# Kernel tuning notes

Hardware: AMD Instinct MI355X
Metric: run time of the kernel (lower is better)

Reference implementation:

```python
import jax, jax.numpy as jnp
import numpy as np

WIDTH, HEIGHT = 96, 72
DIST_COEF = 0.1  # CARLA

# CARLA intrinsics per options_from_source: fx=fy=cx=width/2, cy=height/2
_K = np.array([[48.0, 48.0, 0.0], [36.0, 0.0, 36.0], [1.0, 0.0, 0.0]], dtype=np.float64)
_invK = np.linalg.inv(_K)
_u = np.arange(WIDTH, dtype=np.float64)
_v = np.arange(HEIGHT, dtype=np.float64)
_uu = np.tile(_u, (HEIGHT, 1)).reshape(-1)
_vv = np.repeat(_v, WIDTH)
_uv1 = np.stack([_uu, _vv, np.ones_like(_uu)], axis=0)  # (3, N)
YZ1_GRID = jnp.asarray((_invK @ _uv1).astype(np.float32))  # (3, N)


def setup_inputs() -> dict:
    key = jax.random.key(0)
    k1, k2, k3, k4, k5, k6 = jax.random.split(key, 6)
    B = 1
    # depths strictly positive so the depth>0 mask keeps every pixel (dense, jit-friendly)
    depth1 = jax.random.uniform(k1, (B, 1, HEIGHT, WIDTH), jnp.float32) * 5.0 + 0.1
    depth2 = jax.random.uniform(k2, (B, 1, HEIGHT, WIDTH), jnp.float32) * 5.0 + 0.1
    img1 = jax.random.normal(k3, (B, 3, HEIGHT, WIDTH), jnp.float32)
    img2 = jax.random.normal(k4, (B, 3, HEIGHT, WIDTH), jnp.float32)
    # near-identity rigid-ish transforms (valid homogeneous poses)
    eye = jnp.eye(4, dtype=jnp.float32)[None]
    noise1 = 0.01 * jax.random.normal(k5, (B, 4, 4), jnp.float32)
    noise2 = 0.01 * jax.random.normal(k6, (B, 4, 4), jnp.float32)
    bottom = jnp.zeros((B, 1, 4), jnp.float32).at[:, 0, 3].set(1.0)
    pose1_2 = jnp.concatenate([(eye + noise1)[:, :3, :], bottom], axis=1)
    pose1_2_gt = jnp.concatenate([(eye + noise2)[:, :3, :], bottom], axis=1)
    return {"depth1": depth1, "depth2": depth2, "pose1_2": pose1_2,
            "img1": img1, "img2": img2, "pose1_2_gt": pose1_2_gt}


def _kern_sum(a, b, gram):
    # a: (B,3,N), b: (B,3,M), gram: (B,N,M)
    # sum over n,m of exp(-||a_n - b_m||^2 * dist_coef) * gram[n,m]
    sq = (jnp.sum(a * a, axis=1)[:, :, None]
          + jnp.sum(b * b, axis=1)[:, None, :]
          - 2.0 * jnp.einsum('bcn,bcm->bnm', a, b))
    return jnp.sum(jnp.exp(-sq * DIST_COEF) * gram, axis=(1, 2))  # (B,)


def _transform(pose, xyz):
    # pose: (B,4,4), xyz: (B,3,N) -> rotated+translated points (B,3,N)
    return jnp.einsum('bij,bjn->bin', pose[:, :3, :3], xyz) + pose[:, :3, 3:4]


def reference(depth1, depth2, pose1_2, img1, img2, pose1_2_gt):
    B = depth1.shape[0]
    d1 = depth1.reshape(B, 1, -1)  # (B,1,N)
    d2 = depth2.reshape(B, 1, -1)
    f1 = img1.reshape(B, 3, -1)    # (B,3,N)
    f2 = img2.reshape(B, 3, -1)

    xyz1 = YZ1_GRID[None] * d1     # (B,3,N) back-projected points
    xyz2 = YZ1_GRID[None] * d2
    xyz2_t = _transform(pose1_2, xyz2)
    xyz2_tgt = _transform(pose1_2_gt, xyz2)

    # gramian(..., norm_mode=False, kernalize=False) -> plain feature inner products
    g11 = jnp.einsum('bcn,bcm->bnm', f1, f1)
    g22 = jnp.einsum('bcn,bcm->bnm', f2, f2)
    g12 = jnp.einsum('bcn,bcm->bnm', f1, f2)

    f1_f1 = _kern_sum(xyz1, xyz1, g11)
    f2_f2 = _kern_sum(xyz2_t, xyz2_t, g22)
    f1_f2 = _kern_sum(xyz1, xyz2_t, g12)
    f2_f2_gt = _kern_sum(xyz2_tgt, xyz2_tgt, g22)
    f1_f2_gt = _kern_sum(xyz1, xyz2_tgt, g12)

    inner_neg = f1_f1 + f2_f2 - 2.0 * f1_f2
    inner_neg_gt = f1_f1 + f2_f2_gt - 2.0 * f1_f2_gt
    return jnp.sum(inner_neg / inner_neg_gt)  # scalar, summed over batch
```

## Files before the change

### kernel.cpp

```cpp
#include <hip/hip_runtime.h>

typedef float v2f __attribute__((ext_vector_type(2)));

constexpr int WIDTH  = 96;
constexpr int HEIGHT = 72;
constexpr int NPTS   = WIDTH * HEIGHT;

constexpr int BLOCK  = 128;

constexpr int TT     = 256;
constexpr int T      = NPTS / TT;
constexpr int NPAIR  = T * (T + 1) / 2;
constexpr int MCH    = 64;
constexpr int NCHT   = TT / MCH;
constexpr int NBT    = NPAIR * NCHT;

constexpr int NTILE  = 384;
constexpr int MTILE  = 64;
constexpr int NTB    = NPTS / NTILE;
constexpr int MTB    = NPTS / MTILE;
constexpr int NBF    = NTB * MTB;

constexpr int NBLK   = NBT + NBF;

constexpr int ROWT   = 20;
constexpr int ROWFN  = 8;
constexpr int ROWFM  = 12;

constexpr float KEXP  = -0.14426950408889634f;
constexpr float M2K   = -2.0f * KEXP;

__global__ __launch_bounds__(256) void precompute_kernel(
    const float* __restrict__ depth1, const float* __restrict__ depth2,
    const float* __restrict__ pose,   const float* __restrict__ img1,
    const float* __restrict__ img2,   const float* __restrict__ poseg,
    float* __restrict__ QT, float* __restrict__ QFn, float* __restrict__ QFm)
{
    const int idx = blockIdx.x * 256 + threadIdx.x;

    float R[12], G[12];
#pragma unroll
    for (int i = 0; i < 12; ++i) { R[i] = pose[i]; G[i] = poseg[i]; }

    const int u = idx % WIDTH;
    const int v = idx / WIDTH;
    const float gy = (float)u * (1.0f / 48.0f) - 1.0f;
    const float gz = (float)v * (1.0f / 36.0f) - 1.0f;
    const float d1 = depth1[idx];
    const float d2 = depth2[idx];
    const float x1 = d1, y1 = d1 * gy, z1 = d1 * gz;
    const float x2 = d2, y2 = d2 * gy, z2 = d2 * gz;
    const float xt = R[0] * x2 + R[1] * y2 + R[2]  * z2 + R[3];
    const float yt = R[4] * x2 + R[5] * y2 + R[6]  * z2 + R[7];
    const float zt = R[8] * x2 + R[9] * y2 + R[10] * z2 + R[11];
    const float xg = G[0] * x2 + G[1] * y2 + G[2]  * z2 + G[3];
    const float yg = G[4] * x2 + G[5] * y2 + G[6]  * z2 + G[7];
    const float zg = G[8] * x2 + G[9] * y2 + G[10] * z2 + G[11];

    const float q1 = KEXP * (x1*x1 + y1*y1 + z1*z1);
    const float qt = KEXP * (xt*xt + yt*yt + zt*zt);
    const float qg = KEXP * (xg*xg + yg*yg + zg*zg);
    const float f1a = img1[idx], f1b = img1[NPTS + idx], f1c = img1[2*NPTS + idx];
    const float f2a = img2[idx], f2b = img2[NPTS + idx], f2c = img2[2*NPTS + idx];

    float4* qt_row = (float4*)(QT + (size_t)idx * ROWT);
    qt_row[0] = make_float4(x1, y1, z1, q1);
    qt_row[1] = make_float4(xt, yt, zt, qt);
    qt_row[2] = make_float4(xg, yg, zg, qg);
    qt_row[3] = make_float4(f1a, f1b, f1c, f2a);
    qt_row[4] = make_float4(f2b, f2c, 0.f, 0.f);

    float4* fn_row = (float4*)(QFn + (size_t)idx * ROWFN);
    fn_row[0] = make_float4(M2K * x1, M2K * y1, M2K * z1, q1);
    fn_row[1] = make_float4(f1a, f1b, f1c, 0.f);

    float4* fm_row = (float4*)(QFm + (size_t)idx * ROWFM);
    fm_row[0] = make_float4(xt, yt, zt, qt);
    fm_row[1] = make_float4(xg, yg, zg, qg);
    fm_row[2] = make_float4(f2a, f2b, f2c, 0.f);
}

__global__ __launch_bounds__(BLOCK) void pair_kernel(
    const float* __restrict__ QT,  const float* __restrict__ QFn,
    const float* __restrict__ QFm,
    float* __restrict__ pT, float* __restrict__ pF)
{
    __shared__ float red[2][3];
    const int t = threadIdx.x;

    if (blockIdx.x < NBT) {
        const int pair  = blockIdx.x >> 2;
        const int chunk = blockIdx.x & 3;
        int rem = pair, i = 0;
        while (rem >= T - i) { rem -= T - i; ++i; }
        const int j = i + rem;

        v2f A[18];
        {
            const float4* r0 = (const float4*)(QT + (size_t)(i * TT + t) * ROWT);
            const float4* r1 = (const float4*)(QT + (size_t)(i * TT + BLOCK + t) * ROWT);
#pragma unroll
            for (int g = 0; g < 3; ++g) {
                const float4 w0 = r0[g], w1 = r1[g];
                A[4*g+0].x = M2K*w0.x; A[4*g+0].y = M2K*w1.x;
                A[4*g+1].x = M2K*w0.y; A[4*g+1].y = M2K*w1.y;
                A[4*g+2].x = M2K*w0.z; A[4*g+2].y = M2K*w1.z;
                A[4*g+3].x = w0.w;     A[4*g+3].y = w1.w;
            }
            const float4 w30 = r0[3], w31 = r1[3];
            const float4 w40 = r0[4], w41 = r1[4];
            A[12].x=w30.x; A[12].y=w31.x;  A[13].x=w30.y; A[13].y=w31.y;
            A[14].x=w30.z; A[14].y=w31.z;  A[15].x=w30.w; A[15].y=w31.w;
            A[16].x=w40.x; A[16].y=w41.x;  A[17].x=w40.y; A[17].y=w41.y;
        }

        v2f s0 = {0.f, 0.f}, s1 = s0, s3 = s0;
        const float* __restrict__ q0 =
            QT + (size_t)(j * TT + chunk * MCH) * ROWT;

#pragma unroll 2
        for (int m = 0; m < MCH; ++m) {
            const float* __restrict__ b = q0 + m * ROWT;
            v2f t11 = A[3] + b[3];
            t11 = A[0] * b[0] + t11;
            t11 = A[1] * b[1] + t11;
            t11 = A[2] * b[2] + t11;
            v2f t22 = A[7] + b[7];
            t22 = A[4] * b[4] + t22;
            t22 = A[5] * b[5] + t22;
            t22 = A[6] * b[6] + t22;
            v2f tgg = A[11] + b[11];
            tgg = A[8]  * b[8]  + tgg;
            tgg = A[9]  * b[9]  + tgg;
            tgg = A[10] * b[10] + tgg;
            v2f g11 = A[12] * b[12];
            g11 = A[13] * b[13] + g11;
            g11 = A[14] * b[14] + g11;
            v2f g22 = A[15] * b[15];
            g22 = A[16] * b[16] + g22;
            g22 = A[17] * b[17] + g22;
            v2f e11, e22, egg;
            e11.x = __builtin_amdgcn_exp2f(t11.x);
            e11.y = __builtin_amdgcn_exp2f(t11.y);
            e22.x = __builtin_amdgcn_exp2f(t22.x);
            e22.y = __builtin_amdgcn_exp2f(t22.y);
            egg.x = __builtin_amdgcn_exp2f(tgg.x);
            egg.y = __builtin_amdgcn_exp2f(tgg.y);
            s0 = e11 * g11 + s0;
            s1 = e22 * g22 + s1;
            s3 = egg * g22 + s3;
        }
        const float w = (i == j) ? 1.f : 2.f;
        float r0 = w * (s0.x + s0.y);
        float r1 = w * (s1.x + s1.y);
        float r3 = w * (s3.x + s3.y);

#pragma unroll
        for (int off = 32; off > 0; off >>= 1) {
            r0 += __shfl_down(r0, off);
            r1 += __shfl_down(r1, off);
            r3 += __shfl_down(r3, off);
        }
        const int wave = t >> 6, lane = t & 63;
        if (lane == 0) { red[wave][0]=r0; red[wave][1]=r1; red[wave][2]=r3; }
        __syncthreads();
        if (t == 0) {
            pT[0 * NBT + blockIdx.x] = red[0][0] + red[1][0];
            pT[1 * NBT + blockIdx.x] = red[0][1] + red[1][1];
            pT[2 * NBT + blockIdx.x] = red[0][2] + red[1][2];
        }
    } else {
        const int blk = blockIdx.x - NBT;
        const int bn = blk % NTB;
        const int bm = blk / NTB;

        v2f A2[7];  float A1[7];
        {
            const int n0 = bn * NTILE + t;
            const float4* r0 = (const float4*)(QFn + (size_t)n0 * ROWFN);
            const float4* r1 = (const float4*)(QFn + (size_t)(n0 + BLOCK) * ROWFN);
            const float4* r2 = (const float4*)(QFn + (size_t)(n0 + 2*BLOCK) * ROWFN);
            const float4 a0 = r0[0], a1 = r0[1];
            const float4 c0 = r1[0], c1 = r1[1];
            const float4 d0 = r2[0], d1 = r2[1];
            A2[0].x=a0.x; A2[0].y=c0.x;  A2[1].x=a0.y; A2[1].y=c0.y;
            A2[2].x=a0.z; A2[2].y=c0.z;  A2[3].x=a0.w; A2[3].y=c0.w;
            A2[4].x=a1.x; A2[4].y=c1.x;  A2[5].x=a1.y; A2[5].y=c1.y;
            A2[6].x=a1.z; A2[6].y=c1.z;
            A1[0]=d0.x; A1[1]=d0.y; A1[2]=d0.z; A1[3]=d0.w;
            A1[4]=d1.x; A1[5]=d1.y; A1[6]=d1.z;
        }

        v2f s2v = {0.f, 0.f}, s4v = s2v;
        float s2s = 0.f, s4s = 0.f;
        const float* __restrict__ q0 = QFm + (size_t)(bm * MTILE) * ROWFM;

#pragma unroll 2
        for (int m = 0; m < MTILE; ++m) {
            const float* __restrict__ b = q0 + m * ROWFM;
            v2f t12 = A2[3] + b[3];
            t12 = A2[0] * b[0] + t12;
            t12 = A2[1] * b[1] + t12;
            t12 = A2[2] * b[2] + t12;
            v2f t1g = A2[3] + b[7];
            t1g = A2[0] * b[4] + t1g;
            t1g = A2[1] * b[5] + t1g;
            t1g = A2[2] * b[6] + t1g;
            v2f g12 = A2[4] * b[8];
            g12 = A2[5] * b[9]  + g12;
            g12 = A2[6] * b[10] + g12;
            float u12 = A1[3] + b[3];
            u12 = A1[0] * b[0] + u12;
            u12 = A1[1] * b[1] + u12;
            u12 = A1[2] * b[2] + u12;
            float u1g = A1[3] + b[7];
            u1g = A1[0] * b[4] + u1g;
            u1g = A1[1] * b[5] + u1g;
            u1g = A1[2] * b[6] + u1g;
            float h12 = A1[4] * b[8];
            h12 = A1[5] * b[9]  + h12;
            h12 = A1[6] * b[10] + h12;

            v2f e12, e1g;
            e12.x = __builtin_amdgcn_exp2f(t12.x);
            e12.y = __builtin_amdgcn_exp2f(t12.y);
            e1g.x = __builtin_amdgcn_exp2f(t1g.x);
            e1g.y = __builtin_amdgcn_exp2f(t1g.y);
            const float f12 = __builtin_amdgcn_exp2f(u12);
            const float f1g = __builtin_amdgcn_exp2f(u1g);

            s2v = e12 * g12 + s2v;
            s4v = e1g * g12 + s4v;
            s2s = f12 * h12 + s2s;
            s4s = f1g * h12 + s4s;
        }

        float r2 = s2v.x + s2v.y + s2s;
        float r4 = s4v.x + s4v.y + s4s;
#pragma unroll
        for (int off = 32; off > 0; off >>= 1) {
            r2 += __shfl_down(r2, off);
            r4 += __shfl_down(r4, off);
        }
        const int wave = t >> 6, lane = t & 63;
        if (lane == 0) { red[wave][0] = r2; red[wave][1] = r4; }
        __syncthreads();
        if (t == 0) {
            pF[0 * NBF + blk] = red[0][0] + red[1][0];
            pF[1 * NBF + blk] = red[0][1] + red[1][1];
        }
    }
}

__global__ __launch_bounds__(256) void finalize_kernel(
    const float* __restrict__ pT, const float* __restrict__ pF,
    float* __restrict__ out)
{
    __shared__ double red[4][5];
    double l0 = 0, l1 = 0, l2 = 0, l3 = 0, l4 = 0;
    for (int b = threadIdx.x; b < NBT; b += 256) {
        l0 += pT[0 * NBT + b];
        l1 += pT[1 * NBT + b];
        l3 += pT[2 * NBT + b];
    }
    for (int b = threadIdx.x; b < NBF; b += 256) {
        l2 += pF[0 * NBF + b];
        l4 += pF[1 * NBF + b];
    }
#pragma unroll
    for (int off = 32; off > 0; off >>= 1) {
        l0 += __shfl_down(l0, off);
        l1 += __shfl_down(l1, off);
        l2 += __shfl_down(l2, off);
        l3 += __shfl_down(l3, off);
        l4 += __shfl_down(l4, off);
    }
    const int wave = threadIdx.x >> 6, lane = threadIdx.x & 63;
    if (lane == 0) {
        red[wave][0] = l0; red[wave][1] = l1; red[wave][2] = l2;
        red[wave][3] = l3; red[wave][4] = l4;
    }
    __syncthreads();
    if (threadIdx.x == 0) {
        const double a0 = red[0][0] + red[1][0] + red[2][0] + red[3][0];
        const double a1 = red[0][1] + red[1][1] + red[2][1] + red[3][1];
        const double a2 = red[0][2] + red[1][2] + red[2][2] + red[3][2];
        const double a3 = red[0][3] + red[1][3] + red[2][3] + red[3][3];
        const double a4 = red[0][4] + red[1][4] + red[2][4] + red[3][4];
        const double num = a0 + a1 - 2.0 * a2;
        const double den = a0 + a3 - 2.0 * a4;
        out[0] = (float)(num / den);
    }
}

extern "C" void kernel_launch(void* const* d_in, const int* in_sizes, int n_in,
                              void* d_out, int out_size, void* d_ws, size_t ws_size,
                              hipStream_t stream)
{
    const float* depth1 = (const float*)d_in[0];
    const float* depth2 = (const float*)d_in[1];
    const float* pose   = (const float*)d_in[2];
    const float* img1   = (const float*)d_in[3];
    const float* img2   = (const float*)d_in[4];
    const float* poseg  = (const float*)d_in[5];

    float* QT  = (float*)d_ws;
    float* QFn = QT  + (size_t)NPTS * ROWT;
    float* QFm = QFn + (size_t)NPTS * ROWFN;
    float* pT  = QFm + (size_t)NPTS * ROWFM;
    float* pF  = pT  + 3 * NBT;

    precompute_kernel<<<NPTS / 256, 256, 0, stream>>>(depth1, depth2, pose,
                                                      img1, img2, poseg,
                                                      QT, QFn, QFm);
    pair_kernel<<<NBLK, BLOCK, 0, stream>>>(QT, QFn, QFm, pT, pF);
    finalize_kernel<<<1, 256, 0, stream>>>(pT, pF, (float*)d_out);
}
```

Before: 54.08 us.

## Enlarge per-thread row tiles and reorder cross-term blocks before triangle blocks

Triangle tiles grow from 256 to 384 points, so each thread holds three rows (two packed plus one scalar). Cross-term tiles grow from 384 to 768 points, with three packed row pairs per thread. This raises reuse of each loaded column row and cuts the block count and partial sums. The cross-term blocks now dispatch first, and launch bounds ask for 4 blocks per SIMD. Higher register pressure may lower occupancy or cause spills, and fewer blocks may leave CUs underused.

```diff
diff --git a/kernel.cpp b/kernel.cpp
--- a/kernel.cpp
+++ b/kernel.cpp
@@ -8,20 +8,20 @@
 
 constexpr int BLOCK  = 128;
 
-constexpr int TT     = 256;
+constexpr int NTILE  = 768;
+constexpr int MTILE  = 64;
+constexpr int NTB    = NPTS / NTILE;
+constexpr int MTB    = NPTS / MTILE;
+constexpr int NBF    = NTB * MTB;
+
+constexpr int TT     = 384;
 constexpr int T      = NPTS / TT;
 constexpr int NPAIR  = T * (T + 1) / 2;
 constexpr int MCH    = 64;
 constexpr int NCHT   = TT / MCH;
 constexpr int NBT    = NPAIR * NCHT;
 
-constexpr int NTILE  = 384;
-constexpr int MTILE  = 64;
-constexpr int NTB    = NPTS / NTILE;
-constexpr int MTB    = NPTS / MTILE;
-constexpr int NBF    = NTB * MTB;
-
-constexpr int NBLK   = NBT + NBF;
+constexpr int NBLK   = NBF + NBT;
 
 constexpr int ROWT   = 20;
 constexpr int ROWFN  = 8;
@@ -80,7 +80,7 @@
     fm_row[2] = make_float4(f2a, f2b, f2c, 0.f);
 }
 
-__global__ __launch_bounds__(BLOCK) void pair_kernel(
+__global__ __launch_bounds__(BLOCK, 4) void pair_kernel(
     const float* __restrict__ QT,  const float* __restrict__ QFn,
     const float* __restrict__ QFm,
     float* __restrict__ pT, float* __restrict__ pF)
@@ -88,57 +88,147 @@
     __shared__ float red[2][3];
     const int t = threadIdx.x;
 
-    if (blockIdx.x < NBT) {
-        const int pair  = blockIdx.x >> 2;
-        const int chunk = blockIdx.x & 3;
+    if (blockIdx.x < NBF) {
+        const int blk = blockIdx.x;
+        const int bn = blk % NTB;
+        const int bm = blk / NTB;
+
+        v2f A[3][7];
+#pragma unroll
+        for (int s = 0; s < 3; ++s) {
+            const int n0 = bn * NTILE + s * (2 * BLOCK) + t;
+            const float4* r0 = (const float4*)(QFn + (size_t)n0 * ROWFN);
+            const float4* r1 = (const float4*)(QFn + (size_t)(n0 + BLOCK) * ROWFN);
+            const float4 a0 = r0[0], a1 = r0[1];
+            const float4 c0 = r1[0], c1 = r1[1];
+            A[s][0].x=a0.x; A[s][0].y=c0.x;  A[s][1].x=a0.y; A[s][1].y=c0.y;
+            A[s][2].x=a0.z; A[s][2].y=c0.z;  A[s][3].x=a0.w; A[s][3].y=c0.w;
+            A[s][4].x=a1.x; A[s][4].y=c1.x;  A[s][5].x=a1.y; A[s][5].y=c1.y;
+            A[s][6].x=a1.z; A[s][6].y=c1.z;
+        }
+
+        v2f s2v[3], s4v[3];
+#pragma unroll
+        for (int s = 0; s < 3; ++s) { s2v[s] = v2f{0.f, 0.f}; s4v[s] = v2f{0.f, 0.f}; }
+
+        const float* __restrict__ q0 = QFm + (size_t)(bm * MTILE) * ROWFM;
+#pragma unroll 2
+        for (int m = 0; m < MTILE; ++m) {
+            const float* __restrict__ b = q0 + m * ROWFM;
+#pragma unroll
+            for (int s = 0; s < 3; ++s) {
+                v2f t12 = A[s][3] + b[3];
+                t12 = A[s][0] * b[0] + t12;
+                t12 = A[s][1] * b[1] + t12;
+                t12 = A[s][2] * b[2] + t12;
+                v2f t1g = A[s][3] + b[7];
+                t1g = A[s][0] * b[4] + t1g;
+                t1g = A[s][1] * b[5] + t1g;
+                t1g = A[s][2] * b[6] + t1g;
+                v2f g12 = A[s][4] * b[8];
+                g12 = A[s][5] * b[9]  + g12;
+                g12 = A[s][6] * b[10] + g12;
+                v2f e12, e1g;
+                e12.x = __builtin_amdgcn_exp2f(t12.x);
+                e12.y = __builtin_amdgcn_exp2f(t12.y);
+                e1g.x = __builtin_amdgcn_exp2f(t1g.x);
+                e1g.y = __builtin_amdgcn_exp2f(t1g.y);
+                s2v[s] = e12 * g12 + s2v[s];
+                s4v[s] = e1g * g12 + s4v[s];
+            }
+        }
+
+        float r2 = s2v[0].x + s2v[0].y + s2v[1].x + s2v[1].y + s2v[2].x + s2v[2].y;
+        float r4 = s4v[0].x + s4v[0].y + s4v[1].x + s4v[1].y + s4v[2].x + s4v[2].y;
+#pragma unroll
+        for (int off = 32; off > 0; off >>= 1) {
+            r2 += __shfl_down(r2, off);
+            r4 += __shfl_down(r4, off);
+        }
+        const int wave = t >> 6, lane = t & 63;
+        if (lane == 0) { red[wave][0] = r2; red[wave][1] = r4; }
+        __syncthreads();
+        if (t == 0) {
+            pF[0 * NBF + blk] = red[0][0] + red[1][0];
+            pF[1 * NBF + blk] = red[0][1] + red[1][1];
+        }
+    } else {
+        const int tb    = blockIdx.x - NBF;
+        const int pair  = tb / NCHT;
+        const int chunk = tb % NCHT;
         int rem = pair, i = 0;
         while (rem >= T - i) { rem -= T - i; ++i; }
         const int j = i + rem;
 
-        v2f A[18];
+        v2f Av[18];   float As[18];
         {
             const float4* r0 = (const float4*)(QT + (size_t)(i * TT + t) * ROWT);
             const float4* r1 = (const float4*)(QT + (size_t)(i * TT + BLOCK + t) * ROWT);
+            const float4* r2 = (const float4*)(QT + (size_t)(i * TT + 2 * BLOCK + t) * ROWT);
 #pragma unroll
             for (int g = 0; g < 3; ++g) {
-                const float4 w0 = r0[g], w1 = r1[g];
-                A[4*g+0].x = M2K*w0.x; A[4*g+0].y = M2K*w1.x;
-                A[4*g+1].x = M2K*w0.y; A[4*g+1].y = M2K*w1.y;
-                A[4*g+2].x = M2K*w0.z; A[4*g+2].y = M2K*w1.z;
-                A[4*g+3].x = w0.w;     A[4*g+3].y = w1.w;
+                const float4 w0 = r0[g], w1 = r1[g], w2 = r2[g];
+                Av[4*g+0].x = M2K*w0.x; Av[4*g+0].y = M2K*w1.x; As[4*g+0] = M2K*w2.x;
+                Av[4*g+1].x = M2K*w0.y; Av[4*g+1].y = M2K*w1.y; As[4*g+1] = M2K*w2.y;
+                Av[4*g+2].x = M2K*w0.z; Av[4*g+2].y = M2K*w1.z; As[4*g+2] = M2K*w2.z;
+                Av[4*g+3].x = w0.w;     Av[4*g+3].y = w1.w;     As[4*g+3] = w2.w;
             }
-            const float4 w30 = r0[3], w31 = r1[3];
-            const float4 w40 = r0[4], w41 = r1[4];
-            A[12].x=w30.x; A[12].y=w31.x;  A[13].x=w30.y; A[13].y=w31.y;
-            A[14].x=w30.z; A[14].y=w31.z;  A[15].x=w30.w; A[15].y=w31.w;
-            A[16].x=w40.x; A[16].y=w41.x;  A[17].x=w40.y; A[17].y=w41.y;
-        }
-
-        v2f s0 = {0.f, 0.f}, s1 = s0, s3 = s0;
+            const float4 w30 = r0[3], w31 = r1[3], w32 = r2[3];
+            const float4 w40 = r0[4], w41 = r1[4], w42 = r2[4];
+            Av[12].x=w30.x; Av[12].y=w31.x; As[12]=w32.x;
+            Av[13].x=w30.y; Av[13].y=w31.y; As[13]=w32.y;
+            Av[14].x=w30.z; Av[14].y=w31.z; As[14]=w32.z;
+            Av[15].x=w30.w; Av[15].y=w31.w; As[15]=w32.w;
+            Av[16].x=w40.x; Av[16].y=w41.x; As[16]=w42.x;
+            Av[17].x=w40.y; Av[17].y=w41.y; As[17]=w42.y;
+        }
+
+        v2f s0v = {0.f, 0.f}, s1v = s0v, s3v = s0v;
+        float s0s = 0.f, s1s = 0.f, s3s = 0.f;
         const float* __restrict__ q0 =
             QT + (size_t)(j * TT + chunk * MCH) * ROWT;
 
 #pragma unroll 2
         for (int m = 0; m < MCH; ++m) {
             const float* __restrict__ b = q0 + m * ROWT;
-            v2f t11 = A[3] + b[3];
-            t11 = A[0] * b[0] + t11;
-            t11 = A[1] * b[1] + t11;
-            t11 = A[2] * b[2] + t11;
-            v2f t22 = A[7] + b[7];
-            t22 = A[4] * b[4] + t22;
-            t22 = A[5] * b[5] + t22;
-            t22 = A[6] * b[6] + t22;
-            v2f tgg = A[11] + b[11];
-            tgg = A[8]  * b[8]  + tgg;
-            tgg = A[9]  * b[9]  + tgg;
-            tgg = A[10] * b[10] + tgg;
-            v2f g11 = A[12] * b[12];
-            g11 = A[13] * b[13] + g11;
-            g11 = A[14] * b[14] + g11;
-            v2f g22 = A[15] * b[15];
-            g22 = A[16] * b[16] + g22;
-            g22 = A[17] * b[17] + g22;
+            v2f t11 = Av[3] + b[3];
+            t11 = Av[0] * b[0] + t11;
+            t11 = Av[1] * b[1] + t11;
+            t11 = Av[2] * b[2] + t11;
+            v2f t22 = Av[7] + b[7];
+            t22 = Av[4] * b[4] + t22;
+            t22 = Av[5] * b[5] + t22;
+            t22 = Av[6] * b[6] + t22;
+            v2f tgg = Av[11] + b[11];
+            tgg = Av[8]  * b[8]  + tgg;
+            tgg = Av[9]  * b[9]  + tgg;
+            tgg = Av[10] * b[10] + tgg;
+            v2f g11 = Av[12] * b[12];
+            g11 = Av[13] * b[13] + g11;
+            g11 = Av[14] * b[14] + g11;
+            v2f g22 = Av[15] * b[15];
+            g22 = Av[16] * b[16] + g22;
+            g22 = Av[17] * b[17] + g22;
+
+            float u11 = As[3] + b[3];
+            u11 = As[0] * b[0] + u11;
+            u11 = As[1] * b[1] + u11;
+            u11 = As[2] * b[2] + u11;
+            float u22 = As[7] + b[7];
+            u22 = As[4] * b[4] + u22;
+            u22 = As[5] * b[5] + u22;
+            u22 = As[6] * b[6] + u22;
+            float ugg = As[11] + b[11];
+            ugg = As[8]  * b[8]  + ugg;
+            ugg = As[9]  * b[9]  + ugg;
+            ugg = As[10] * b[10] + ugg;
+            float h11 = As[12] * b[12];
+            h11 = As[13] * b[13] + h11;
+            h11 = As[14] * b[14] + h11;
+            float h22 = As[15] * b[15];
+            h22 = As[16] * b[16] + h22;
+            h22 = As[17] * b[17] + h22;
+
             v2f e11, e22, egg;
             e11.x = __builtin_amdgcn_exp2f(t11.x);
             e11.y = __builtin_amdgcn_exp2f(t11.y);
@@ -146,14 +236,21 @@
             e22.y = __builtin_amdgcn_exp2f(t22.y);
             egg.x = __builtin_amdgcn_exp2f(tgg.x);
             egg.y = __builtin_amdgcn_exp2f(tgg.y);
-            s0 = e11 * g11 + s0;
-            s1 = e22 * g22 + s1;
-            s3 = egg * g22 + s3;
+            const float f11 = __builtin_amdgcn_exp2f(u11);
+            const float f22 = __builtin_amdgcn_exp2f(u22);
+            const float fgg = __builtin_amdgcn_exp2f(ugg);
+
+            s0v = e11 * g11 + s0v;
+            s1v = e22 * g22 + s1v;
+            s3v = egg * g22 + s3v;
+            s0s = f11 * h11 + s0s;
+            s1s = f22 * h22 + s1s;
+            s3s = fgg * h22 + s3s;
         }
         const float w = (i == j) ? 1.f : 2.f;
-        float r0 = w * (s0.x + s0.y);
-        float r1 = w * (s1.x + s1.y);
-        float r3 = w * (s3.x + s3.y);
+        float r0 = w * (s0v.x + s0v.y + s0s);
+        float r1 = w * (s1v.x + s1v.y + s1s);
+        float r3 = w * (s3v.x + s3v.y + s3s);
 
 #pragma unroll
         for (int off = 32; off > 0; off >>= 1) {
@@ -165,89 +262,9 @@
         if (lane == 0) { red[wave][0]=r0; red[wave][1]=r1; red[wave][2]=r3; }
         __syncthreads();
         if (t == 0) {
-            pT[0 * NBT + blockIdx.x] = red[0][0] + red[1][0];
-            pT[1 * NBT + blockIdx.x] = red[0][1] + red[1][1];
-            pT[2 * NBT + blockIdx.x] = red[0][2] + red[1][2];
-        }
-    } else {
-        const int blk = blockIdx.x - NBT;
-        const int bn = blk % NTB;
-        const int bm = blk / NTB;
-
-        v2f A2[7];  float A1[7];
-        {
-            const int n0 = bn * NTILE + t;
-            const float4* r0 = (const float4*)(QFn + (size_t)n0 * ROWFN);
-            const float4* r1 = (const float4*)(QFn + (size_t)(n0 + BLOCK) * ROWFN);
-            const float4* r2 = (const float4*)(QFn + (size_t)(n0 + 2*BLOCK) * ROWFN);
-            const float4 a0 = r0[0], a1 = r0[1];
-            const float4 c0 = r1[0], c1 = r1[1];
-            const float4 d0 = r2[0], d1 = r2[1];
-            A2[0].x=a0.x; A2[0].y=c0.x;  A2[1].x=a0.y; A2[1].y=c0.y;
-            A2[2].x=a0.z; A2[2].y=c0.z;  A2[3].x=a0.w; A2[3].y=c0.w;
-            A2[4].x=a1.x; A2[4].y=c1.x;  A2[5].x=a1.y; A2[5].y=c1.y;
-            A2[6].x=a1.z; A2[6].y=c1.z;
-            A1[0]=d0.x; A1[1]=d0.y; A1[2]=d0.z; A1[3]=d0.w;
-            A1[4]=d1.x; A1[5]=d1.y; A1[6]=d1.z;
-        }
-
-        v2f s2v = {0.f, 0.f}, s4v = s2v;
-        float s2s = 0.f, s4s = 0.f;
-        const float* __restrict__ q0 = QFm + (size_t)(bm * MTILE) * ROWFM;
-
-#pragma unroll 2
-        for (int m = 0; m < MTILE; ++m) {
-            const float* __restrict__ b = q0 + m * ROWFM;
-            v2f t12 = A2[3] + b[3];
-            t12 = A2[0] * b[0] + t12;
-            t12 = A2[1] * b[1] + t12;
-            t12 = A2[2] * b[2] + t12;
-            v2f t1g = A2[3] + b[7];
-            t1g = A2[0] * b[4] + t1g;
-            t1g = A2[1] * b[5] + t1g;
-            t1g = A2[2] * b[6] + t1g;
-            v2f g12 = A2[4] * b[8];
-            g12 = A2[5] * b[9]  + g12;
-            g12 = A2[6] * b[10] + g12;
-            float u12 = A1[3] + b[3];
-            u12 = A1[0] * b[0] + u12;
-            u12 = A1[1] * b[1] + u12;
-            u12 = A1[2] * b[2] + u12;
-            float u1g = A1[3] + b[7];
-            u1g = A1[0] * b[4] + u1g;
-            u1g = A1[1] * b[5] + u1g;
-            u1g = A1[2] * b[6] + u1g;
-            float h12 = A1[4] * b[8];
-            h12 = A1[5] * b[9]  + h12;
-            h12 = A1[6] * b[10] + h12;
-
-            v2f e12, e1g;
-            e12.x = __builtin_amdgcn_exp2f(t12.x);
-            e12.y = __builtin_amdgcn_exp2f(t12.y);
-            e1g.x = __builtin_amdgcn_exp2f(t1g.x);
-            e1g.y = __builtin_amdgcn_exp2f(t1g.y);
-            const float f12 = __builtin_amdgcn_exp2f(u12);
-            const float f1g = __builtin_amdgcn_exp2f(u1g);
-
-            s2v = e12 * g12 + s2v;
-            s4v = e1g * g12 + s4v;
-            s2s = f12 * h12 + s2s;
-            s4s = f1g * h12 + s4s;
-        }
-
-        float r2 = s2v.x + s2v.y + s2s;
-        float r4 = s4v.x + s4v.y + s4s;
-#pragma unroll
-        for (int off = 32; off > 0; off >>= 1) {
-            r2 += __shfl_down(r2, off);
-            r4 += __shfl_down(r4, off);
-        }
-        const int wave = t >> 6, lane = t & 63;
-        if (lane == 0) { red[wave][0] = r2; red[wave][1] = r4; }
-        __syncthreads();
-        if (t == 0) {
-            pF[0 * NBF + blk] = red[0][0] + red[1][0];
-            pF[1 * NBF + blk] = red[0][1] + red[1][1];
+            pT[0 * NBT + tb] = red[0][0] + red[1][0];
+            pT[1 * NBT + tb] = red[0][1] + red[1][1];
+            pT[2 * NBT + tb] = red[0][2] + red[1][2];
         }
     }
 }
```

After: 53.71 us. No clear change (-0.7%).
